# Optimization experiments

Measured on AMD Instinct MI355X. Metric: run time of the kernel, lower is better.

The kernel has to match this reference:

```python
import jax, jax.numpy as jnp
import numpy as np

NEG_SLOPE = 0.2  # LeakyReLU slope
B, F_BAND, T = 32, 128, 2048
HID, NCLASS = 256, 64


def _corrcoef(m):
    # m: [..., n, k] -> correlation matrix between rows, [..., n, n] (torch.corrcoef semantics)
    m = m - m.mean(axis=-1, keepdims=True)
    c = jnp.einsum('...ik,...jk->...ij', m, m)
    d = jnp.sqrt(jnp.clip(jnp.diagonal(c, axis1=-2, axis2=-1), 0.0, None))
    corr = c / (d[..., :, None] * d[..., None, :])
    return jnp.clip(corr, -1.0, 1.0)


def _leaky(x):
    return jnp.where(x >= 0, x, NEG_SLOPE * x)


def setup_inputs() -> dict:
    key = jax.random.key(0)
    ks = jax.random.split(key, 9)
    def lin(k, fin, fout):
        return jax.random.normal(k, (fin, fout), dtype=jnp.float32) / np.sqrt(fin)
    x = jax.random.normal(ks[0], (B, F_BAND, T), dtype=jnp.float32)
    return {
        'x': x,
        'W1': lin(ks[1], T, HID),      'b1': jnp.zeros((HID,), jnp.float32),
        'W2': lin(ks[2], HID, HID),    'b2': jnp.zeros((HID,), jnp.float32),
        'W3': lin(ks[3], HID, NCLASS), 'b3': jnp.zeros((NCLASS,), jnp.float32),
        'W4': lin(ks[4], NCLASS, NCLASS), 'b4': jnp.zeros((NCLASS,), jnp.float32),
    }


def reference(x, W1, b1, W2, b2, W3, b3, W4, b4):
    Bs, Fb, Tt = x.shape
    node = Fb
    step = node  # typeFeature=2 -> overlap=0
    A = len(range(0, Tt - node, step))  # number of time windows
    # windows: x[:, :, a*node:(a+1)*node] -> [B, A, F, node]
    xw = x[:, :, :A * node].reshape(Bs, Fb, A, node).transpose(0, 2, 1, 3)
    # torch.corrcoef(fi.T): rows = window-column index (node), variables over F bands
    adj = _corrcoef(jnp.swapaxes(xw, -1, -2))  # [B, A, node, node] == [B, A, F, F]
    adj = jnp.nan_to_num((adj + 1.0) * 0.5)
    # gnnBlock vectorized over all A windows (x broadcast along A). Dropout is eval-mode no-op.
    h = _leaky(jnp.einsum('banm,bmt->bant', adj, x) @ W1 + b1)    # [B,A,F,HID]
    h = _leaky(jnp.einsum('banm,bamh->banh', adj, h) @ W2 + b2)   # [B,A,F,HID]
    xa = _leaky(jnp.einsum('banm,bamh->banh', adj, h) @ W3 + b3)  # [B,A,F,C]
    # typeFeature==2 head: mean over nodes, corrcoef over windows, gc4
    xa = xa.mean(axis=2)         # [B, A, C]
    adj2 = _corrcoef(xa)         # [B, A, A]
    out = _leaky(jnp.einsum('bij,bjc->bic', adj2, xa) @ W4 + b4)  # [B, A, C]
    # max over dim=1; GradMultiply with grad_mul=1.0 is identity in fwd
    return out.max(axis=1)       # [B, C]
```

## Files before the change

kernel.cpp:

```cpp
#include <hip/hip_runtime.h>


typedef float f32x4 __attribute__((ext_vector_type(4)));
typedef __bf16 bf16x8 __attribute__((ext_vector_type(8)));
typedef unsigned short u16x4 __attribute__((ext_vector_type(4)));
typedef unsigned short u16x8 __attribute__((ext_vector_type(8)));

__device__ inline unsigned short f2b(float f) {
  unsigned int u = __float_as_uint(f);
  unsigned int r = u + 0x7fffu + ((u >> 16) & 1u);
  return (unsigned short)(r >> 16);
}
__device__ inline float leaky(float v) { return v >= 0.f ? v : 0.2f * v; }

#define SWZ(k, r) ((k) ^ (((r) & 7) << 3))

__global__ __launch_bounds__(512) void k_front(const float* __restrict__ x,
                                               const float* __restrict__ W1,
                                               const float* __restrict__ W2,
                                               const float* __restrict__ W3,
                                               unsigned short* __restrict__ W2T,
                                               unsigned short* __restrict__ W3T,
                                               unsigned short* __restrict__ xT,
                                               unsigned short* __restrict__ XW1T) {
  __shared__ __align__(16) char lds[16640 + 8192 + 16384];
  float (*tW)[65] = reinterpret_cast<float (*)[65]>(lds);
  unsigned short* sW = reinterpret_cast<unsigned short*>(lds + 16640);
  unsigned short (*sX)[64 * 64] =
      reinterpret_cast<unsigned short (*)[64 * 64]>(lds + 16640 + 8192);
  const int bid = blockIdx.x, tid = threadIdx.x;
  const int r = tid >> 3, c8 = (tid & 7) * 8;

  if (bid < 20) {
    const float* src;
    unsigned short* dst;
    int K, N, k0, n0;
    if (bid < 16) { src = W2; dst = W2T; K = 256; N = 256; k0 = (bid >> 2) * 64; n0 = (bid & 3) * 64; }
    else          { src = W3; dst = W3T; K = 256; N = 64;  k0 = (bid - 16) * 64; n0 = 0; }
#pragma unroll
    for (int j = 0; j < 8; ++j) tW[r][c8 + j] = src[(size_t)(k0 + r) * N + n0 + c8 + j];
    __syncthreads();
    u16x8 s;
#pragma unroll
    for (int j = 0; j < 8; ++j) s[j] = f2b(tW[c8 + j][r]);
    *(u16x8*)&dst[(size_t)(n0 + r) * K + k0 + c8] = s;
  } else if (bid < 276) {
    const int i = bid - 20;
    const int b = i >> 3, q = i & 7;
    const int hid0 = (q >> 1) * 64, f0 = (q & 1) * 64;
    const int w = tid >> 6, lane = tid & 63;
    const int l15 = lane & 15, l4 = lane >> 4;
    const float* xb = x + ((size_t)b * 128 + f0) * 2048;
    f32x4 xr0, xr1, wr0, wr1;
    f32x4 acc[2] = {};

    auto LOADX = [&](int kb) {
      xr0 = *(const f32x4*)&xb[(size_t)r * 2048 + kb * 64 + c8];
      xr1 = *(const f32x4*)&xb[(size_t)r * 2048 + kb * 64 + c8 + 4];
    };
    auto LOADW = [&](int kb) {
      wr0 = *(const f32x4*)&W1[(size_t)(kb * 64 + r) * 256 + hid0 + c8];
      wr1 = *(const f32x4*)&W1[(size_t)(kb * 64 + r) * 256 + hid0 + c8 + 4];
    };
    auto STOREX = [&](int buf) {
      u16x8 s;
#pragma unroll
      for (int j = 0; j < 8; ++j) s[j] = f2b(j < 4 ? xr0[j] : xr1[j - 4]);
      *(u16x8*)&sX[buf][r * 64 + SWZ(c8, r)] = s;
    };
    auto STOREW = [&]() {
#pragma unroll
      for (int j = 0; j < 4; ++j) { tW[r][c8 + j] = wr0[j]; tW[r][c8 + 4 + j] = wr1[j]; }
    };
    auto PACKW = [&]() {
      u16x8 s;
#pragma unroll
      for (int j = 0; j < 8; ++j) s[j] = f2b(tW[c8 + j][r]);
      *(u16x8*)&sW[r * 64 + SWZ(c8, r)] = s;
    };

    LOADX(0); LOADW(0);
    STOREX(0); STOREW();
    __syncthreads();
    PACKW();
    __syncthreads();
    for (int kb = 0; kb < 32; ++kb) {
      if (kb < 31) { LOADX(kb + 1); LOADW(kb + 1); }
      const int buf = kb & 1;
#pragma unroll
      for (int ks = 0; ks < 2; ++ks) {
        int ar = (w & 3) * 16 + l15;
        bf16x8 af = *(const bf16x8*)&sW[ar * 64 + SWZ(ks * 32 + l4 * 8, ar)];
#pragma unroll
        for (int nt = 0; nt < 2; ++nt) {
          int br = (w >> 2) * 32 + nt * 16 + l15;
          bf16x8 bf = *(const bf16x8*)&sX[buf][br * 64 + SWZ(ks * 32 + l4 * 8, br)];
          acc[nt] = __builtin_amdgcn_mfma_f32_16x16x32_bf16(af, bf, acc[nt], 0, 0, 0);
        }
      }
      if (kb < 31) {
        STOREX(buf ^ 1);
        STOREW();
        __syncthreads();
        PACKW();
        __syncthreads();
      }
    }
    unsigned short* dst = XW1T + (size_t)b * 256 * 128;
#pragma unroll
    for (int nt = 0; nt < 2; ++nt)
#pragma unroll
      for (int rr = 0; rr < 4; ++rr) {
        int p = hid0 + (w & 3) * 16 + l4 * 4 + rr;
        int f = f0 + (w >> 2) * 32 + nt * 16 + l15;
        dst[p * 128 + f] = f2b(acc[nt][rr]);
      }
  } else {
    const int i = bid - 276;
    const int b = i >> 6, rem = i & 63;
    const int t0 = (rem >> 1) * 64, f0 = (rem & 1) * 64;
    const float* xb = x + ((size_t)b * 128 + f0) * 2048 + t0;
    f32x4 v0 = *(const f32x4*)&xb[(size_t)r * 2048 + c8];
    f32x4 v1 = *(const f32x4*)&xb[(size_t)r * 2048 + c8 + 4];
#pragma unroll
    for (int j = 0; j < 4; ++j) { tW[r][c8 + j] = v0[j]; tW[r][c8 + 4 + j] = v1[j]; }
    __syncthreads();
    u16x8 s;
#pragma unroll
    for (int j = 0; j < 8; ++j) s[j] = f2b(tW[c8 + j][r]);
    *(u16x8*)&xT[((size_t)b * 2048 + t0 + r) * 128 + f0 + c8] = s;
  }
}

__global__ __launch_bounds__(512) void k_chain(
    const unsigned short* __restrict__ xT, const unsigned short* __restrict__ XW1T,
    const unsigned short* __restrict__ W2T, const unsigned short* __restrict__ W3T,
    const float* __restrict__ b1g, const float* __restrict__ b2g,
    const float* __restrict__ b3g, float* __restrict__ gXa) {
  __shared__ __align__(16) unsigned short R0[128 * 128];
  __shared__ __align__(16) unsigned short R1[128 * 128];
  __shared__ float fS[256];

  const int tid = threadIdx.x;
  const int w = tid >> 6, lane = tid & 63;
  const int l15 = lane & 15, l4 = lane >> 4;
  const int ridx = (blockIdx.x & 7) * 60 + (blockIdx.x >> 3);
  const int b = ridx / 15, a = ridx % 15;
  const int m0 = w * 16;
  const unsigned short* XWb = XW1T + (size_t)b * 256 * 128;
  const float inv128 = 1.f / 128.f;

  const unsigned short* src = xT + ((size_t)b * 2048 + (size_t)a * 128) * 128;
#pragma unroll 1
  for (int it = 0; it < 4; ++it) {
    int tt = tid + it * 512;
    int j = tt >> 4, f8 = (tt & 15) * 8;
    *(u16x8*)&R1[j * 128 + SWZ(f8, j)] = *(const u16x8*)&src[j * 128 + f8];
  }
  __syncthreads();

  bf16x8 afw[4];
#pragma unroll
  for (int ks = 0; ks < 4; ++ks) {
    int ar = m0 + l15;
    afw[ks] = *(const bf16x8*)&R1[ar * 128 + SWZ(ks * 32 + l4 * 8, ar)];
  }
  bf16x8 ones;
#pragma unroll
  for (int q = 0; q < 8; ++q) ones[q] = (__bf16)1.0f;
  f32x4 sacc = {}, dacc = {};
#pragma unroll
  for (int ks = 0; ks < 4; ++ks) {
    sacc = __builtin_amdgcn_mfma_f32_16x16x32_bf16(afw[ks], ones, sacc, 0, 0, 0);
    dacc = __builtin_amdgcn_mfma_f32_16x16x32_bf16(afw[ks], afw[ks], dacc, 0, 0, 0);
  }
#pragma unroll
  for (int r = 0; r < 4; ++r) {
    if (l15 == 0) fS[m0 + l4 * 4 + r] = sacc[r];
    if (l15 == l4 * 4 + r)
      fS[128 + m0 + l4 * 4 + r] = dacc[r] - sacc[r] * sacc[r] * inv128;
  }
  __syncthreads();

  float div[4];
#pragma unroll
  for (int r = 0; r < 4; ++r) {
    float d = fS[128 + m0 + l4 * 4 + r];
    div[r] = d > 0.f ? __frsqrt_rn(d) : 0.f;
  }
#pragma unroll 1
  for (int nt = 0; nt < 8; ++nt) {
    int col = nt * 16 + l15;
    f32x4 c = {};
#pragma unroll
    for (int ks = 0; ks < 4; ++ks) {
      bf16x8 bf = *(const bf16x8*)&R1[col * 128 + SWZ(ks * 32 + l4 * 8, col)];
      c = __builtin_amdgcn_mfma_f32_16x16x32_bf16(afw[ks], bf, c, 0, 0, 0);
    }
    float fc = fS[col];
    float dc = fS[128 + col];
    float djv = dc > 0.f ? __frsqrt_rn(dc) : 0.f;
    u16x4 pk;
#pragma unroll
    for (int r = 0; r < 4; ++r) {
      float v = (c[r] - sacc[r] * fc * inv128) * div[r] * djv;
      v = fminf(1.f, fmaxf(-1.f, v));
      v = 0.5f * v + 0.5f;
      if (div[r] == 0.f || djv == 0.f) v = 0.f;
      pk[r] = f2b(v);
    }
    *(u16x4*)&R0[col * 128 + SWZ(m0 + l4 * 4, col)] = pk;
  }
  __syncthreads();

  bf16x8 afj[4];
#pragma unroll
  for (int ks = 0; ks < 4; ++ks)
    afj[ks] = *(const bf16x8*)&R0[(m0 + l15) * 128 + SWZ(ks * 32 + l4 * 8, m0 + l15)];

#pragma unroll 1
  for (int half = 0; half < 2; ++half) {
    unsigned short* Rd = half ? R0 : R1;
    const unsigned short* Bbase = &XWb[(size_t)half * 128 * 128 + l4 * 8];
    bf16x8 bpf[4];
#pragma unroll
    for (int ks = 0; ks < 4; ++ks)
      bpf[ks] = *(const bf16x8*)&Bbase[(size_t)l15 * 128 + ks * 32];
#pragma unroll 1
    for (int nt = 0; nt < 8; ++nt) {
      bf16x8 bc[4];
#pragma unroll
      for (int ks = 0; ks < 4; ++ks) bc[ks] = bpf[ks];
      if (nt < 7) {
#pragma unroll
        for (int ks = 0; ks < 4; ++ks)
          bpf[ks] = *(const bf16x8*)&Bbase[(size_t)((nt + 1) * 16 + l15) * 128 + ks * 32];
      }
      f32x4 acc = {};
#pragma unroll
      for (int ks = 0; ks < 4; ++ks)
        acc = __builtin_amdgcn_mfma_f32_16x16x32_bf16(afj[ks], bc[ks], acc, 0, 0, 0);
      float bias = b1g[half * 128 + nt * 16 + l15];
#pragma unroll
      for (int r = 0; r < 4; ++r) {
        int row = m0 + l4 * 4 + r;
        Rd[row * 128 + SWZ(nt * 16 + l15, row)] = f2b(leaky(acc[r] + bias));
      }
    }
  }
  __syncthreads();

  f32x4 u2[2][8] = {};
  {
    const unsigned short* A0 = &W2T[(size_t)(w * 32 + l15) * 256 + l4 * 8];
    const unsigned short* A1 = &W2T[(size_t)(w * 32 + 16 + l15) * 256 + l4 * 8];
    bf16x8 a0p = *(const bf16x8*)&A0[0];
    bf16x8 a1p = *(const bf16x8*)&A1[0];
#pragma unroll 1
    for (int ks = 0; ks < 8; ++ks) {
      bf16x8 a0 = a0p, a1 = a1p;
      if (ks < 7) {
        a0p = *(const bf16x8*)&A0[(ks + 1) * 32];
        a1p = *(const bf16x8*)&A1[(ks + 1) * 32];
      }
      const unsigned short* Rs = (ks < 4) ? R1 : R0;
      int kk = (ks & 3) * 32 + l4 * 8;
#pragma unroll
      for (int nt = 0; nt < 8; ++nt) {
        int br = nt * 16 + l15;
        bf16x8 bf = *(const bf16x8*)&Rs[br * 128 + SWZ(kk, br)];
        u2[0][nt] = __builtin_amdgcn_mfma_f32_16x16x32_bf16(a0, bf, u2[0][nt], 0, 0, 0);
        u2[1][nt] = __builtin_amdgcn_mfma_f32_16x16x32_bf16(a1, bf, u2[1][nt], 0, 0, 0);
      }
    }
  }
  __syncthreads();

#pragma unroll
  for (int mt = 0; mt < 2; ++mt)
#pragma unroll
    for (int nt = 0; nt < 8; ++nt)
#pragma unroll
      for (int r = 0; r < 4; ++r) {
        int grow = w * 32 + mt * 16 + l4 * 4 + r;
        int col = nt * 16 + l15;
        unsigned short* Rd = (grow < 128) ? R0 : R1;
        int lr = grow & 127;
        Rd[lr * 128 + SWZ(col, lr)] = f2b(u2[mt][nt][r]);
      }
  __syncthreads();

  f32x4 h2acc[16];
#pragma unroll
  for (int nt = 0; nt < 16; ++nt) h2acc[nt] = f32x4{0.f, 0.f, 0.f, 0.f};
#pragma unroll
  for (int ks = 0; ks < 4; ++ks)
#pragma unroll
    for (int nt = 0; nt < 16; ++nt) {
      int brl = (nt & 7) * 16 + l15;
      const unsigned short* Rs = (nt < 8) ? R0 : R1;
      bf16x8 bf = *(const bf16x8*)&Rs[brl * 128 + SWZ(ks * 32 + l4 * 8, brl)];
      h2acc[nt] = __builtin_amdgcn_mfma_f32_16x16x32_bf16(afj[ks], bf, h2acc[nt], 0, 0, 0);
    }
  __syncthreads();

#pragma unroll
  for (int nt = 0; nt < 16; ++nt) {
    float bias = b2g[nt * 16 + l15];
#pragma unroll
    for (int r = 0; r < 4; ++r) {
      int row = m0 + l4 * 4 + r;
      int coll = (nt & 7) * 16 + l15;
      unsigned short* Rd = (nt < 8) ? R0 : R1;
      Rd[row * 128 + SWZ(coll, row)] = f2b(leaky(h2acc[nt][r] + bias));
    }
  }
  const int mrow = (w >> 1) * 16, ntb = (w & 1) * 4;
  bf16x8 a3f[8];
#pragma unroll
  for (int ks = 0; ks < 8; ++ks)
    a3f[ks] = *(const bf16x8*)&W3T[(size_t)(mrow + l15) * 256 + ks * 32 + l4 * 8];
  __syncthreads();

  f32x4 u3[4] = {};
#pragma unroll
  for (int kh = 0; kh < 2; ++kh) {
    const unsigned short* Rs = kh ? R1 : R0;
#pragma unroll
    for (int ks = 0; ks < 4; ++ks) {
#pragma unroll
      for (int nti = 0; nti < 4; ++nti) {
        int br = (ntb + nti) * 16 + l15;
        bf16x8 bf = *(const bf16x8*)&Rs[br * 128 + SWZ(ks * 32 + l4 * 8, br)];
        u3[nti] = __builtin_amdgcn_mfma_f32_16x16x32_bf16(a3f[kh * 4 + ks], bf, u3[nti], 0, 0, 0);
      }
    }
  }
  __syncthreads();

#pragma unroll
  for (int nti = 0; nti < 4; ++nti)
#pragma unroll
    for (int r = 0; r < 4; ++r) {
      int grow = mrow + l4 * 4 + r;
      int col = (ntb + nti) * 16 + l15;
      R0[grow * 128 + SWZ(col, grow)] = f2b(u3[nti][r]);
    }
  __syncthreads();

  {
    float* pf = reinterpret_cast<float*>(R1);
#pragma unroll 1
    for (int nt = 0; nt < 4; ++nt) {
      f32x4 acc = {};
      int br = nt * 16 + l15;
#pragma unroll
      for (int ks = 0; ks < 4; ++ks) {
        bf16x8 bf = *(const bf16x8*)&R0[br * 128 + SWZ(ks * 32 + l4 * 8, br)];
        acc = __builtin_amdgcn_mfma_f32_16x16x32_bf16(afj[ks], bf, acc, 0, 0, 0);
      }
      float bias = b3g[br];
      float v = 0.f;
#pragma unroll
      for (int r = 0; r < 4; ++r) v += leaky(acc[r] + bias);
      v += __shfl_xor(v, 16);
      v += __shfl_xor(v, 32);
      if (l4 == 0) pf[w * 64 + br] = v;
    }
  }
  __syncthreads();
  if (tid < 64) {
    const float* pf = reinterpret_cast<const float*>(R1);
    float s = 0.f;
#pragma unroll
    for (int gg = 0; gg < 8; ++gg) s += pf[gg * 64 + tid];
    gXa[((size_t)b * 15 + a) * 64 + tid] = s * (1.f / 128.f);
  }
}

__global__ __launch_bounds__(256) void k_head(const float* __restrict__ gXa,
                                              const float* __restrict__ W4,
                                              const float* __restrict__ b4,
                                              float* __restrict__ out) {
  __shared__ float xb[15 * 64];
  __shared__ float c2[15 * 16];
  __shared__ float mu[15];
  __shared__ float dinv[15];
  __shared__ float yy[15 * 64];
  __shared__ float zz[15 * 64];
  const int b = blockIdx.x;
  const int tid = threadIdx.x;
  for (int e = tid; e < 960; e += 256) xb[e] = gXa[(size_t)b * 960 + e];
  __syncthreads();
  if (tid < 15) {
    float s = 0.f;
    for (int c = 0; c < 64; ++c) s += xb[tid * 64 + c];
    mu[tid] = s * (1.f / 64.f);
  }
  __syncthreads();
  if (tid < 225) {
    int p = tid / 15, q = tid % 15;
    float s = 0.f;
    for (int c = 0; c < 64; ++c)
      s += (xb[p * 64 + c] - mu[p]) * (xb[q * 64 + c] - mu[q]);
    c2[p * 16 + q] = s;
  }
  __syncthreads();
  if (tid < 15) {
    float d = c2[tid * 16 + tid];
    dinv[tid] = d > 0.f ? (1.f / sqrtf(d)) : 0.f;
  }
  __syncthreads();
  if (tid < 225) {
    int p = tid / 15, q = tid % 15;
    float v = c2[p * 16 + q] * dinv[p] * dinv[q];
    v = fminf(1.f, fmaxf(-1.f, v));
    if (dinv[p] == 0.f || dinv[q] == 0.f) v = 0.f;
    c2[p * 16 + q] = v;
  }
  __syncthreads();
  for (int e = tid; e < 960; e += 256) {
    int p = e >> 6, c = e & 63;
    float s = 0.f;
    for (int q = 0; q < 15; ++q) s += c2[p * 16 + q] * xb[q * 64 + c];
    yy[e] = s;
  }
  __syncthreads();
  for (int e = tid; e < 960; e += 256) {
    int p = e >> 6, c = e & 63;
    float s = b4[c];
    for (int k = 0; k < 64; ++k) s += yy[p * 64 + k] * W4[k * 64 + c];
    zz[e] = leaky(s);
  }
  __syncthreads();
  if (tid < 64) {
    float m = -INFINITY;
    for (int p = 0; p < 15; ++p) m = fmaxf(m, zz[p * 64 + tid]);
    out[(size_t)b * 64 + tid] = m;
  }
}

extern "C" void kernel_launch(void* const* d_in, const int* in_sizes, int n_in,
                              void* d_out, int out_size, void* d_ws, size_t ws_size,
                              hipStream_t stream) {
  const float* x  = (const float*)d_in[0];
  const float* W1 = (const float*)d_in[1];
  const float* b1 = (const float*)d_in[2];
  const float* W2 = (const float*)d_in[3];
  const float* b2 = (const float*)d_in[4];
  const float* W3 = (const float*)d_in[5];
  const float* b3 = (const float*)d_in[6];
  const float* W4 = (const float*)d_in[7];
  const float* b4 = (const float*)d_in[8];
  float* out = (float*)d_out;

  char* ws = (char*)d_ws;
  unsigned short* xT   = (unsigned short*)ws;
  unsigned short* XW1T = (unsigned short*)(ws + 16777216);
  unsigned short* W2T  = (unsigned short*)(ws + 18874368);
  unsigned short* W3T  = (unsigned short*)(ws + 19005440);
  float* gXa           = (float*)(ws + 19038208);

  k_front<<<2324, 512, 0, stream>>>(x, W1, W2, W3, W2T, W3T, xT, XW1T);
  k_chain<<<480, 512, 0, stream>>>(xT, XW1T, W2T, W3T, b1, b2, b3, gXa);
  k_head<<<32, 256, 0, stream>>>(gXa, W4, b4, out);
}
```

Baseline: 111.8 us.

## Process two (batch, window) pairs per k_chain block to reuse weight fragments

```diff
diff --git a/kernel.cpp b/kernel.cpp
--- a/kernel.cpp
+++ b/kernel.cpp
@@ -137,184 +137,201 @@
     const unsigned short* __restrict__ W2T, const unsigned short* __restrict__ W3T,
     const float* __restrict__ b1g, const float* __restrict__ b2g,
     const float* __restrict__ b3g, float* __restrict__ gXa) {
-  __shared__ __align__(16) unsigned short R0[128 * 128];
-  __shared__ __align__(16) unsigned short R1[128 * 128];
-  __shared__ float fS[256];
+  __shared__ __align__(16) unsigned short R0[2][128 * 128];
+  __shared__ __align__(16) unsigned short R1[2][128 * 128];
+  __shared__ float fS[2][256];
 
   const int tid = threadIdx.x;
   const int w = tid >> 6, lane = tid & 63;
   const int l15 = lane & 15, l4 = lane >> 4;
-  const int ridx = (blockIdx.x & 7) * 60 + (blockIdx.x >> 3);
-  const int b = ridx / 15, a = ridx % 15;
+  const int pid = (blockIdx.x & 7) * 30 + (blockIdx.x >> 3);
+  int bb[2], aa[2];
+  bb[0] = pid / 15;         aa[0] = pid % 15;
+  bb[1] = (pid + 240) / 15; aa[1] = (pid + 240) % 15;
   const int m0 = w * 16;
-  const unsigned short* XWb = XW1T + (size_t)b * 256 * 128;
   const float inv128 = 1.f / 128.f;
 
-  const unsigned short* src = xT + ((size_t)b * 2048 + (size_t)a * 128) * 128;
-#pragma unroll 1
-  for (int it = 0; it < 4; ++it) {
-    int tt = tid + it * 512;
-    int j = tt >> 4, f8 = (tt & 15) * 8;
-    *(u16x8*)&R1[j * 128 + SWZ(f8, j)] = *(const u16x8*)&src[j * 128 + f8];
-  }
-  __syncthreads();
-
-  bf16x8 afw[4];
-#pragma unroll
-  for (int ks = 0; ks < 4; ++ks) {
-    int ar = m0 + l15;
-    afw[ks] = *(const bf16x8*)&R1[ar * 128 + SWZ(ks * 32 + l4 * 8, ar)];
-  }
+#pragma unroll
+  for (int v = 0; v < 2; ++v) {
+    const unsigned short* src = xT + ((size_t)bb[v] * 2048 + (size_t)aa[v] * 128) * 128;
+#pragma unroll 1
+    for (int it = 0; it < 4; ++it) {
+      int tt = tid + it * 512;
+      int j = tt >> 4, f8 = (tt & 15) * 8;
+      *(u16x8*)&R1[v][j * 128 + SWZ(f8, j)] = *(const u16x8*)&src[j * 128 + f8];
+    }
+  }
+  __syncthreads();
+
+  bf16x8 afw[2][4];
+  f32x4 sacc[2], dacc[2];
   bf16x8 ones;
 #pragma unroll
   for (int q = 0; q < 8; ++q) ones[q] = (__bf16)1.0f;
-  f32x4 sacc = {}, dacc = {};
-#pragma unroll
-  for (int ks = 0; ks < 4; ++ks) {
-    sacc = __builtin_amdgcn_mfma_f32_16x16x32_bf16(afw[ks], ones, sacc, 0, 0, 0);
-    dacc = __builtin_amdgcn_mfma_f32_16x16x32_bf16(afw[ks], afw[ks], dacc, 0, 0, 0);
-  }
-#pragma unroll
-  for (int r = 0; r < 4; ++r) {
-    if (l15 == 0) fS[m0 + l4 * 4 + r] = sacc[r];
-    if (l15 == l4 * 4 + r)
-      fS[128 + m0 + l4 * 4 + r] = dacc[r] - sacc[r] * sacc[r] * inv128;
-  }
-  __syncthreads();
-
-  float div[4];
-#pragma unroll
-  for (int r = 0; r < 4; ++r) {
-    float d = fS[128 + m0 + l4 * 4 + r];
-    div[r] = d > 0.f ? __frsqrt_rn(d) : 0.f;
-  }
+#pragma unroll
+  for (int v = 0; v < 2; ++v) {
+#pragma unroll
+    for (int ks = 0; ks < 4; ++ks) {
+      int ar = m0 + l15;
+      afw[v][ks] = *(const bf16x8*)&R1[v][ar * 128 + SWZ(ks * 32 + l4 * 8, ar)];
+    }
+    sacc[v] = f32x4{0.f, 0.f, 0.f, 0.f};
+    dacc[v] = f32x4{0.f, 0.f, 0.f, 0.f};
+#pragma unroll
+    for (int ks = 0; ks < 4; ++ks) {
+      sacc[v] = __builtin_amdgcn_mfma_f32_16x16x32_bf16(afw[v][ks], ones, sacc[v], 0, 0, 0);
+      dacc[v] = __builtin_amdgcn_mfma_f32_16x16x32_bf16(afw[v][ks], afw[v][ks], dacc[v], 0, 0, 0);
+    }
+#pragma unroll
+    for (int r = 0; r < 4; ++r) {
+      if (l15 == 0) fS[v][m0 + l4 * 4 + r] = sacc[v][r];
+      if (l15 == l4 * 4 + r)
+        fS[v][128 + m0 + l4 * 4 + r] = dacc[v][r] - sacc[v][r] * sacc[v][r] * inv128;
+    }
+  }
+  __syncthreads();
+
+  float div_[2][4];
+#pragma unroll
+  for (int v = 0; v < 2; ++v)
+#pragma unroll
+    for (int r = 0; r < 4; ++r) {
+      float d = fS[v][128 + m0 + l4 * 4 + r];
+      div_[v][r] = d > 0.f ? __frsqrt_rn(d) : 0.f;
+    }
 #pragma unroll 1
   for (int nt = 0; nt < 8; ++nt) {
     int col = nt * 16 + l15;
-    f32x4 c = {};
-#pragma unroll
-    for (int ks = 0; ks < 4; ++ks) {
-      bf16x8 bf = *(const bf16x8*)&R1[col * 128 + SWZ(ks * 32 + l4 * 8, col)];
-      c = __builtin_amdgcn_mfma_f32_16x16x32_bf16(afw[ks], bf, c, 0, 0, 0);
-    }
-    float fc = fS[col];
-    float dc = fS[128 + col];
-    float djv = dc > 0.f ? __frsqrt_rn(dc) : 0.f;
-    u16x4 pk;
-#pragma unroll
-    for (int r = 0; r < 4; ++r) {
-      float v = (c[r] - sacc[r] * fc * inv128) * div[r] * djv;
-      v = fminf(1.f, fmaxf(-1.f, v));
-      v = 0.5f * v + 0.5f;
-      if (div[r] == 0.f || djv == 0.f) v = 0.f;
-      pk[r] = f2b(v);
-    }
-    *(u16x4*)&R0[col * 128 + SWZ(m0 + l4 * 4, col)] = pk;
-  }
-  __syncthreads();
-
-  bf16x8 afj[4];
+#pragma unroll
+    for (int v = 0; v < 2; ++v) {
+      f32x4 c = {};
+#pragma unroll
+      for (int ks = 0; ks < 4; ++ks) {
+        bf16x8 bf = *(const bf16x8*)&R1[v][col * 128 + SWZ(ks * 32 + l4 * 8, col)];
+        c = __builtin_amdgcn_mfma_f32_16x16x32_bf16(afw[v][ks], bf, c, 0, 0, 0);
+      }
+      float fc = fS[v][col];
+      float dc = fS[v][128 + col];
+      float djv = dc > 0.f ? __frsqrt_rn(dc) : 0.f;
+      u16x4 pk;
+#pragma unroll
+      for (int r = 0; r < 4; ++r) {
+        float val = (c[r] - sacc[v][r] * fc * inv128) * div_[v][r] * djv;
+        val = fminf(1.f, fmaxf(-1.f, val));
+        val = 0.5f * val + 0.5f;
+        if (div_[v][r] == 0.f || djv == 0.f) val = 0.f;
+        pk[r] = f2b(val);
+      }
+      *(u16x4*)&R0[v][col * 128 + SWZ(m0 + l4 * 4, col)] = pk;
+    }
+  }
+  __syncthreads();
+
+  bf16x8 afj[2][4];
+#pragma unroll
+  for (int v = 0; v < 2; ++v)
+#pragma unroll
+    for (int ks = 0; ks < 4; ++ks)
+      afj[v][ks] = *(const bf16x8*)&R0[v][(m0 + l15) * 128 + SWZ(ks * 32 + l4 * 8, m0 + l15)];
+
+  const unsigned short* XWb0 = XW1T + (size_t)bb[0] * 256 * 128;
+  const unsigned short* XWb1 = XW1T + (size_t)bb[1] * 256 * 128;
+#pragma unroll 1
+  for (int half = 0; half < 2; ++half) {
+#pragma unroll 1
+    for (int nt = 0; nt < 8; ++nt) {
+      float bias = b1g[half * 128 + nt * 16 + l15];
+#pragma unroll
+      for (int v = 0; v < 2; ++v) {
+        const unsigned short* Bp =
+            (v ? XWb1 : XWb0) + (size_t)(half * 128 + nt * 16 + l15) * 128 + l4 * 8;
+        f32x4 acc = {};
+#pragma unroll
+        for (int ks = 0; ks < 4; ++ks) {
+          bf16x8 bf = *(const bf16x8*)&Bp[ks * 32];
+          acc = __builtin_amdgcn_mfma_f32_16x16x32_bf16(afj[v][ks], bf, acc, 0, 0, 0);
+        }
+        unsigned short* Rd = half ? R0[v] : R1[v];
+#pragma unroll
+        for (int r = 0; r < 4; ++r) {
+          int row = m0 + l4 * 4 + r;
+          Rd[row * 128 + SWZ(nt * 16 + l15, row)] = f2b(leaky(acc[r] + bias));
+        }
+      }
+    }
+  }
+  __syncthreads();
+
+  f32x4 u2[2][2][8] = {};
+  {
+#pragma unroll 1
+    for (int ks = 0; ks < 8; ++ks) {
+      bf16x8 a0 = *(const bf16x8*)&W2T[(size_t)(w * 32 + l15) * 256 + ks * 32 + l4 * 8];
+      bf16x8 a1 = *(const bf16x8*)&W2T[(size_t)(w * 32 + 16 + l15) * 256 + ks * 32 + l4 * 8];
+      int kk = (ks & 3) * 32 + l4 * 8;
+#pragma unroll
+      for (int v = 0; v < 2; ++v) {
+        const unsigned short* Rs = (ks < 4) ? R1[v] : R0[v];
+#pragma unroll
+        for (int nt = 0; nt < 8; ++nt) {
+          int br = nt * 16 + l15;
+          bf16x8 bf = *(const bf16x8*)&Rs[br * 128 + SWZ(kk, br)];
+          u2[v][0][nt] = __builtin_amdgcn_mfma_f32_16x16x32_bf16(a0, bf, u2[v][0][nt], 0, 0, 0);
+          u2[v][1][nt] = __builtin_amdgcn_mfma_f32_16x16x32_bf16(a1, bf, u2[v][1][nt], 0, 0, 0);
+        }
+      }
+    }
+  }
+  __syncthreads();
+
+#pragma unroll
+  for (int v = 0; v < 2; ++v)
+#pragma unroll
+    for (int mt = 0; mt < 2; ++mt)
+#pragma unroll
+      for (int nt = 0; nt < 8; ++nt)
+#pragma unroll
+        for (int r = 0; r < 4; ++r) {
+          int grow = w * 32 + mt * 16 + l4 * 4 + r;
+          int col = nt * 16 + l15;
+          unsigned short* Rd = (grow < 128) ? R0[v] : R1[v];
+          int lr = grow & 127;
+          Rd[lr * 128 + SWZ(col, lr)] = f2b(u2[v][mt][nt][r]);
+        }
+  __syncthreads();
+
+  f32x4 h2[2][16];
+#pragma unroll
+  for (int v = 0; v < 2; ++v)
+#pragma unroll
+    for (int nt = 0; nt < 16; ++nt) h2[v][nt] = f32x4{0.f, 0.f, 0.f, 0.f};
 #pragma unroll
   for (int ks = 0; ks < 4; ++ks)
-    afj[ks] = *(const bf16x8*)&R0[(m0 + l15) * 128 + SWZ(ks * 32 + l4 * 8, m0 + l15)];
-
-#pragma unroll 1
-  for (int half = 0; half < 2; ++half) {
-    unsigned short* Rd = half ? R0 : R1;
-    const unsigned short* Bbase = &XWb[(size_t)half * 128 * 128 + l4 * 8];
-    bf16x8 bpf[4];
-#pragma unroll
-    for (int ks = 0; ks < 4; ++ks)
-      bpf[ks] = *(const bf16x8*)&Bbase[(size_t)l15 * 128 + ks * 32];
-#pragma unroll 1
-    for (int nt = 0; nt < 8; ++nt) {
-      bf16x8 bc[4];
-#pragma unroll
-      for (int ks = 0; ks < 4; ++ks) bc[ks] = bpf[ks];
-      if (nt < 7) {
-#pragma unroll
-        for (int ks = 0; ks < 4; ++ks)
-          bpf[ks] = *(const bf16x8*)&Bbase[(size_t)((nt + 1) * 16 + l15) * 128 + ks * 32];
-      }
-      f32x4 acc = {};
-#pragma unroll
-      for (int ks = 0; ks < 4; ++ks)
-        acc = __builtin_amdgcn_mfma_f32_16x16x32_bf16(afj[ks], bc[ks], acc, 0, 0, 0);
-      float bias = b1g[half * 128 + nt * 16 + l15];
+#pragma unroll
+    for (int nt = 0; nt < 16; ++nt) {
+      int brl = (nt & 7) * 16 + l15;
+#pragma unroll
+      for (int v = 0; v < 2; ++v) {
+        const unsigned short* Rs = (nt < 8) ? R0[v] : R1[v];
+        bf16x8 bf = *(const bf16x8*)&Rs[brl * 128 + SWZ(ks * 32 + l4 * 8, brl)];
+        h2[v][nt] = __builtin_amdgcn_mfma_f32_16x16x32_bf16(afj[v][ks], bf, h2[v][nt], 0, 0, 0);
+      }
+    }
+  __syncthreads();
+
+#pragma unroll
+  for (int v = 0; v < 2; ++v)
+#pragma unroll
+    for (int nt = 0; nt < 16; ++nt) {
+      float bias = b2g[nt * 16 + l15];
 #pragma unroll
       for (int r = 0; r < 4; ++r) {
         int row = m0 + l4 * 4 + r;
-        Rd[row * 128 + SWZ(nt * 16 + l15, row)] = f2b(leaky(acc[r] + bias));
-      }
-    }
-  }
-  __syncthreads();
-
-  f32x4 u2[2][8] = {};
-  {
-    const unsigned short* A0 = &W2T[(size_t)(w * 32 + l15) * 256 + l4 * 8];
-    const unsigned short* A1 = &W2T[(size_t)(w * 32 + 16 + l15) * 256 + l4 * 8];
-    bf16x8 a0p = *(const bf16x8*)&A0[0];
-    bf16x8 a1p = *(const bf16x8*)&A1[0];
-#pragma unroll 1
-    for (int ks = 0; ks < 8; ++ks) {
-      bf16x8 a0 = a0p, a1 = a1p;
-      if (ks < 7) {
-        a0p = *(const bf16x8*)&A0[(ks + 1) * 32];
-        a1p = *(const bf16x8*)&A1[(ks + 1) * 32];
-      }
-      const unsigned short* Rs = (ks < 4) ? R1 : R0;
-      int kk = (ks & 3) * 32 + l4 * 8;
-#pragma unroll
-      for (int nt = 0; nt < 8; ++nt) {
-        int br = nt * 16 + l15;
-        bf16x8 bf = *(const bf16x8*)&Rs[br * 128 + SWZ(kk, br)];
-        u2[0][nt] = __builtin_amdgcn_mfma_f32_16x16x32_bf16(a0, bf, u2[0][nt], 0, 0, 0);
-        u2[1][nt] = __builtin_amdgcn_mfma_f32_16x16x32_bf16(a1, bf, u2[1][nt], 0, 0, 0);
-      }
-    }
-  }
-  __syncthreads();
-
-#pragma unroll
-  for (int mt = 0; mt < 2; ++mt)
-#pragma unroll
-    for (int nt = 0; nt < 8; ++nt)
-#pragma unroll
-      for (int r = 0; r < 4; ++r) {
-        int grow = w * 32 + mt * 16 + l4 * 4 + r;
-        int col = nt * 16 + l15;
-        unsigned short* Rd = (grow < 128) ? R0 : R1;
-        int lr = grow & 127;
-        Rd[lr * 128 + SWZ(col, lr)] = f2b(u2[mt][nt][r]);
-      }
-  __syncthreads();
-
-  f32x4 h2acc[16];
-#pragma unroll
-  for (int nt = 0; nt < 16; ++nt) h2acc[nt] = f32x4{0.f, 0.f, 0.f, 0.f};
-#pragma unroll
-  for (int ks = 0; ks < 4; ++ks)
-#pragma unroll
-    for (int nt = 0; nt < 16; ++nt) {
-      int brl = (nt & 7) * 16 + l15;
-      const unsigned short* Rs = (nt < 8) ? R0 : R1;
-      bf16x8 bf = *(const bf16x8*)&Rs[brl * 128 + SWZ(ks * 32 + l4 * 8, brl)];
-      h2acc[nt] = __builtin_amdgcn_mfma_f32_16x16x32_bf16(afj[ks], bf, h2acc[nt], 0, 0, 0);
-    }
-  __syncthreads();
-
-#pragma unroll
-  for (int nt = 0; nt < 16; ++nt) {
-    float bias = b2g[nt * 16 + l15];
-#pragma unroll
-    for (int r = 0; r < 4; ++r) {
-      int row = m0 + l4 * 4 + r;
-      int coll = (nt & 7) * 16 + l15;
-      unsigned short* Rd = (nt < 8) ? R0 : R1;
-      Rd[row * 128 + SWZ(coll, row)] = f2b(leaky(h2acc[nt][r] + bias));
-    }
-  }
+        int coll = (nt & 7) * 16 + l15;
+        unsigned short* Rd = (nt < 8) ? R0[v] : R1[v];
+        Rd[row * 128 + SWZ(coll, row)] = f2b(leaky(h2[v][nt][r] + bias));
+      }
+    }
   const int mrow = (w >> 1) * 16, ntb = (w & 1) * 4;
   bf16x8 a3f[8];
 #pragma unroll
@@ -322,59 +339,65 @@
     a3f[ks] = *(const bf16x8*)&W3T[(size_t)(mrow + l15) * 256 + ks * 32 + l4 * 8];
   __syncthreads();
 
-  f32x4 u3[4] = {};
+  f32x4 u3[2][4] = {};
 #pragma unroll
   for (int kh = 0; kh < 2; ++kh) {
-    const unsigned short* Rs = kh ? R1 : R0;
 #pragma unroll
     for (int ks = 0; ks < 4; ++ks) {
 #pragma unroll
       for (int nti = 0; nti < 4; ++nti) {
         int br = (ntb + nti) * 16 + l15;
-        bf16x8 bf = *(const bf16x8*)&Rs[br * 128 + SWZ(ks * 32 + l4 * 8, br)];
-        u3[nti] = __builtin_amdgcn_mfma_f32_16x16x32_bf16(a3f[kh * 4 + ks], bf, u3[nti], 0, 0, 0);
-      }
-    }
-  }
-  __syncthreads();
-
-#pragma unroll
-  for (int nti = 0; nti < 4; ++nti)
-#pragma unroll
-    for (int r = 0; r < 4; ++r) {
-      int grow = mrow + l4 * 4 + r;
-      int col = (ntb + nti) * 16 + l15;
-      R0[grow * 128 + SWZ(col, grow)] = f2b(u3[nti][r]);
-    }
-  __syncthreads();
-
-  {
-    float* pf = reinterpret_cast<float*>(R1);
-#pragma unroll 1
-    for (int nt = 0; nt < 4; ++nt) {
+#pragma unroll
+        for (int v = 0; v < 2; ++v) {
+          const unsigned short* Rs = kh ? R1[v] : R0[v];
+          bf16x8 bf = *(const bf16x8*)&Rs[br * 128 + SWZ(ks * 32 + l4 * 8, br)];
+          u3[v][nti] = __builtin_amdgcn_mfma_f32_16x16x32_bf16(a3f[kh * 4 + ks], bf, u3[v][nti], 0, 0, 0);
+        }
+      }
+    }
+  }
+  __syncthreads();
+
+#pragma unroll
+  for (int v = 0; v < 2; ++v)
+#pragma unroll
+    for (int nti = 0; nti < 4; ++nti)
+#pragma unroll
+      for (int r = 0; r < 4; ++r) {
+        int grow = mrow + l4 * 4 + r;
+        int col = (ntb + nti) * 16 + l15;
+        R0[v][grow * 128 + SWZ(col, grow)] = f2b(u3[v][nti][r]);
+      }
+  __syncthreads();
+
+#pragma unroll 1
+  for (int nt = 0; nt < 4; ++nt) {
+    int br = nt * 16 + l15;
+    float bias = b3g[br];
+#pragma unroll
+    for (int v = 0; v < 2; ++v) {
       f32x4 acc = {};
-      int br = nt * 16 + l15;
 #pragma unroll
       for (int ks = 0; ks < 4; ++ks) {
-        bf16x8 bf = *(const bf16x8*)&R0[br * 128 + SWZ(ks * 32 + l4 * 8, br)];
-        acc = __builtin_amdgcn_mfma_f32_16x16x32_bf16(afj[ks], bf, acc, 0, 0, 0);
-      }
-      float bias = b3g[br];
-      float v = 0.f;
-#pragma unroll
-      for (int r = 0; r < 4; ++r) v += leaky(acc[r] + bias);
-      v += __shfl_xor(v, 16);
-      v += __shfl_xor(v, 32);
-      if (l4 == 0) pf[w * 64 + br] = v;
-    }
-  }
-  __syncthreads();
-  if (tid < 64) {
-    const float* pf = reinterpret_cast<const float*>(R1);
+        bf16x8 bf = *(const bf16x8*)&R0[v][br * 128 + SWZ(ks * 32 + l4 * 8, br)];
+        acc = __builtin_amdgcn_mfma_f32_16x16x32_bf16(afj[v][ks], bf, acc, 0, 0, 0);
+      }
+      float s = 0.f;
+#pragma unroll
+      for (int r = 0; r < 4; ++r) s += leaky(acc[r] + bias);
+      s += __shfl_xor(s, 16);
+      s += __shfl_xor(s, 32);
+      if (l4 == 0) reinterpret_cast<float*>(R1[v])[w * 64 + br] = s;
+    }
+  }
+  __syncthreads();
+  if (tid < 128) {
+    int v = tid >> 6, c = tid & 63;
+    const float* pf = reinterpret_cast<const float*>(R1[v]);
     float s = 0.f;
 #pragma unroll
-    for (int gg = 0; gg < 8; ++gg) s += pf[gg * 64 + tid];
-    gXa[((size_t)b * 15 + a) * 64 + tid] = s * (1.f / 128.f);
+    for (int gg = 0; gg < 8; ++gg) s += pf[gg * 64 + c];
+    gXa[((size_t)bb[v] * 15 + aa[v]) * 64 + c] = s * inv128;
   }
 }
 
@@ -462,6 +485,6 @@
   float* gXa           = (float*)(ws + 19038208);
 
   k_front<<<2324, 512, 0, stream>>>(x, W1, W2, W3, W2T, W3T, xT, XW1T);
-  k_chain<<<480, 512, 0, stream>>>(xT, XW1T, W2T, W3T, b1, b2, b3, gXa);
+  k_chain<<<240, 512, 0, stream>>>(xT, XW1T, W2T, W3T, b1, b2, b3, gXa);
   k_head<<<32, 256, 0, stream>>>(gXa, W4, b4, out);
 }
```

Result: faster. 108.4 us (-3.1%).
